# Optimization experiments

Measured on AMD Instinct MI355X. Metric: run time of the kernel, lower is better.

## Reference

```python
import jax, jax.numpy as jnp
import numpy as np

C = 512
HEADS = 8
B, H, W = 2, 64, 64


def setup_inputs() -> dict:
    key = jax.random.key(0)
    k1, k2, k3, k4, k5 = jax.random.split(key, 5)
    s = 1.0 / np.sqrt(C)
    return {
        "hidden_states": jax.random.normal(k1, (B, C, H, W), dtype=jnp.float32),
        "qkv_w": jax.random.normal(k2, (3 * C, C), dtype=jnp.float32) * s,
        "qkv_b": jax.random.normal(k3, (3 * C,), dtype=jnp.float32) * 0.02,
        "proj_w": jax.random.normal(k4, (C, C), dtype=jnp.float32) * s,
        "proj_b": jax.random.normal(k5, (C,), dtype=jnp.float32) * 0.02,
    }


def reference(hidden_states, qkv_w, qkv_b, proj_w, proj_b):
    b, c, h, w = hidden_states.shape
    n = h * w  # sequence length
    heads = HEADS
    dim_head = c // heads
    scale = dim_head ** -0.5

    x = hidden_states.reshape(b, c, n)  # [b, c, n]
    # 1x1 conv1d == matmul over channel dim
    qkv = jnp.einsum("oc,bcn->bon", qkv_w, x) + qkv_b[None, :, None]  # [b, 3c, n]
    q, k, v = jnp.split(qkv, 3, axis=1)
    # [b, heads, dim_head, n] -> [b, heads, n, dim_head]
    def split_heads(t):
        return t.reshape(b, heads, dim_head, n).transpose(0, 1, 3, 2)
    q, k, v = split_heads(q), split_heads(k), split_heads(v)

    attn = jnp.einsum("bhqd,bhkd->bhqk", q, k) * scale  # [b, heads, n, n]
    attn = jax.nn.softmax(attn, axis=-1)
    out = jnp.einsum("bhqk,bhkd->bhqd", attn, v)  # [b, heads, n, dim_head]
    out = out.transpose(0, 1, 3, 2).reshape(b, c, n)  # [b, c, n]
    out = jnp.einsum("oc,bcn->bon", proj_w, out) + proj_b[None, :, None]
    return out  # [b, c, h*w] (matches torch module, no reshape back)
```

## Files before the change

### kernel.cpp

```cpp
#include <hip/hip_runtime.h>


typedef __attribute__((ext_vector_type(8))) short s16x8;
typedef __attribute__((ext_vector_type(4))) float f32x4;
typedef __attribute__((ext_vector_type(16))) float f32x16;
typedef __attribute__((ext_vector_type(4))) unsigned short u16x4;
typedef __attribute__((ext_vector_type(2))) unsigned u32x2;
typedef __attribute__((ext_vector_type(4))) unsigned u32x4;

__device__ __forceinline__ unsigned short f2bf(float f) {
  unsigned u = __builtin_bit_cast(unsigned, f);
  u += 0x7fffu + ((u >> 16) & 1u);
  return (unsigned short)(u >> 16);
}

__device__ __forceinline__ float bf2f(short s) {
  return __builtin_bit_cast(float, ((unsigned)(unsigned short)s) << 16);
}

__device__ __forceinline__ unsigned cvt_pk_bf16(float lo, float hi) {
  unsigned r;
  asm("v_cvt_pk_bf16_f32 %0, %1, %2" : "=v"(r) : "v"(lo), "v"(hi));
  return r;
}

__global__ __launch_bounds__(256) void prep_weights(
    const float* __restrict__ qkv_w, const float* __restrict__ proj_w,
    short* __restrict__ wq, short* __restrict__ wp) {
  int t = blockIdx.x * 256 + threadIdx.x;
  const int NQ = 1536 * 512 / 4;
  if (t < NQ) {
    float4 v = ((const float4*)qkv_w)[t];
    u16x4 o; o[0] = f2bf(v.x); o[1] = f2bf(v.y); o[2] = f2bf(v.z); o[3] = f2bf(v.w);
    ((u16x4*)wq)[t] = o;
  } else {
    int t2 = t - NQ;
    float4 v = ((const float4*)proj_w)[t2];
    u16x4 o; o[0] = f2bf(v.x); o[1] = f2bf(v.y); o[2] = f2bf(v.z); o[3] = f2bf(v.w);
    ((u16x4*)wp)[t2] = o;
  }
}

__global__ __launch_bounds__(256) void prep_transpose(
    const float* __restrict__ x, short* __restrict__ xt) {
  __shared__ short TL[64 * 72];
  const int b = blockIdx.z, c0 = blockIdx.y * 64, n0 = blockIdx.x * 64;
  const int t = threadIdx.x;
  const int cr = t >> 4, n4 = (t & 15) * 4;
#pragma unroll
  for (int i = 0; i < 4; i++) {
    int c = cr + i * 16;
    float4 v = *(const float4*)(x + ((size_t)(b * 512 + c0 + c)) * 4096 + n0 + n4);
    TL[(n4 + 0) * 72 + c] = (short)f2bf(v.x);
    TL[(n4 + 1) * 72 + c] = (short)f2bf(v.y);
    TL[(n4 + 2) * 72 + c] = (short)f2bf(v.z);
    TL[(n4 + 3) * 72 + c] = (short)f2bf(v.w);
  }
  __syncthreads();
  const int n = t >> 2;
#pragma unroll
  for (int s2 = 0; s2 < 2; s2++) {
    int s = (t & 3) * 2 + s2;
    s16x8 v = *(const s16x8*)&TL[n * 72 + s * 8];
    *(s16x8*)(xt + ((size_t)(b * 4096 + n0 + n)) * 512 + c0 + s * 8) = v;
  }
}

__global__ __launch_bounds__(256) void qkv_gemm(
    const short* __restrict__ wq, const short* __restrict__ xt,
    const float* __restrict__ qkv_b,
    short* __restrict__ qkbuf,
    short* __restrict__ vbuf) {
  __shared__ short Al[128 * 40];
  __shared__ short Bl[128 * 40];
  const int b = blockIdx.z;
  const int m0 = blockIdx.y * 128, n0 = blockIdx.x * 128;
  const bool swapped = (blockIdx.y < 8);
  const int t = threadIdx.x, lane = t & 63, wid = t >> 6;
  const int wr = wid >> 1, wc = wid & 1;
  const int srow = t >> 1, scol = (t & 1) * 16;
  const short* gA = wq + (size_t)(m0 + srow) * 512 + scol;
  const short* gB = xt + ((size_t)(b * 4096 + n0 + srow)) * 512 + scol;
  short* lA = &Al[srow * 40 + scol];
  short* lB = &Bl[srow * 40 + scol];
  const short* As = swapped ? Bl : Al;
  const short* Bs = swapped ? Al : Bl;
  f32x4 acc[4][4] = {};
  for (int ks = 0; ks < 16; ks++) {
    *(s16x8*)lA       = *(const s16x8*)(gA + ks * 32);
    *(s16x8*)(lA + 8) = *(const s16x8*)(gA + ks * 32 + 8);
    *(s16x8*)lB       = *(const s16x8*)(gB + ks * 32);
    *(s16x8*)(lB + 8) = *(const s16x8*)(gB + ks * 32 + 8);
    __syncthreads();
    s16x8 af[4], bf[4];
#pragma unroll
    for (int i = 0; i < 4; i++) {
      af[i] = *(const s16x8*)&As[(wr * 64 + i * 16 + (lane & 15)) * 40 + ((lane >> 4) << 3)];
      bf[i] = *(const s16x8*)&Bs[(wc * 64 + i * 16 + (lane & 15)) * 40 + ((lane >> 4) << 3)];
    }
#pragma unroll
    for (int i = 0; i < 4; i++)
#pragma unroll
      for (int j = 0; j < 4; j++)
        acc[i][j] = __builtin_amdgcn_mfma_f32_16x16x32_bf16(af[i], bf[j], acc[i][j], 0, 0, 0);
    __syncthreads();
  }
  if (!swapped) {
#pragma unroll
    for (int i = 0; i < 4; i++)
#pragma unroll
      for (int r = 0; r < 4; r++) {
        int orow = m0 + wr * 64 + i * 16 + ((lane >> 4) << 2) + r;
        float bias = qkv_b[orow];
#pragma unroll
        for (int j = 0; j < 4; j++) {
          int ncol = n0 + wc * 64 + j * 16 + (lane & 15);
          vbuf[((size_t)(b * 512 + orow - 1024)) * 4096 + ncol] = (short)f2bf(acc[i][j][r] + bias);
        }
      }
  } else {
    const float qs = (m0 < 512) ? 0.18033688f : 1.0f;
#pragma unroll
    for (int j = 0; j < 4; j++) {
      int ocol = m0 + wc * 64 + j * 16 + (lane & 15);
      float bias = qkv_b[ocol];
#pragma unroll
      for (int i = 0; i < 4; i++)
#pragma unroll
        for (int r = 0; r < 4; r++) {
          int nrow = n0 + wr * 64 + i * 16 + ((lane >> 4) << 2) + r;
          qkbuf[((size_t)(b * 4096 + nrow)) * 1024 + ocol] = (short)f2bf((acc[i][j][r] + bias) * qs);
        }
    }
  }
}

__global__ __launch_bounds__(256) void flash_attn(
    const short* __restrict__ qkbuf, const short* __restrict__ vbuf,
    short* __restrict__ opart,
    float* __restrict__ mlbuf) {
  __shared__ short Kl[64 * 64];
  __shared__ short Vl[64 * 64];
  const int t = threadIdx.x, lane = t & 63, wid = t >> 6;
  const int hi = lane >> 5, q32 = lane & 31;
  const int j = blockIdx.x;
  const int lid = ((j & 7) << 7) + (j >> 3);
  const int bh = lid >> 6, b = bh >> 3, h = bh & 7;
  const int rest = lid & 63;
  const int qc = rest >> 1, half = rest & 1;
  const int qb = qc * 128 + wid * 32;
  const int kt0 = half * 32;

  s16x8 qf[4];
  {
    const short* qrow = qkbuf + ((size_t)(b * 4096 + qb + q32)) * 1024 + h * 64 + hi * 8;
#pragma unroll
    for (int dc = 0; dc < 4; dc++) qf[dc] = *(const s16x8*)(qrow + dc * 16);
  }

  f32x16 oacc[2] = {};
  float m = -__builtin_inff();
  float l = 0.f;

  const int srow = t >> 2;
  const int swz = (srow & 7) << 4;
  const int o0 = ((t & 3) * 32) ^ swz;
  const int o1 = ((t & 3) * 32 + 16) ^ swz;
  const short* gK = qkbuf + ((size_t)(b * 4096 + kt0 * 64 + srow)) * 1024 + 512 + h * 64 + (t & 3) * 16;
  const short* gV = vbuf + ((size_t)(b * 512 + h * 64 + srow)) * 4096 + kt0 * 64 + (t & 3) * 16;
  char* lKrow = (char*)&Kl[srow * 64];
  char* lVrow = (char*)&Vl[srow * 64];

  s16x8 pk0 = *(const s16x8*)gK, pk1 = *(const s16x8*)(gK + 8);
  s16x8 pv0 = *(const s16x8*)gV, pv1 = *(const s16x8*)(gV + 8);

  for (int kt = 0; kt < 32; kt++) {
    *(s16x8*)(lKrow + o0) = pk0;  *(s16x8*)(lKrow + o1) = pk1;
    *(s16x8*)(lVrow + o0) = pv0;  *(s16x8*)(lVrow + o1) = pv1;
    __syncthreads();
    if (kt < 31) {
      const short* nK = gK + (size_t)(kt + 1) * 64 * 1024;
      const short* nV = gV + (kt + 1) * 64;
      pk0 = *(const s16x8*)nK;  pk1 = *(const s16x8*)(nK + 8);
      pv0 = *(const s16x8*)nV;  pv1 = *(const s16x8*)(nV + 8);
    }
#pragma unroll
    for (int kb = 0; kb < 2; kb++) {
      f32x16 st = {};
      const int krow = kb * 32 + q32;
      const int ksw = (krow & 7) << 4;
#pragma unroll
      for (int dc = 0; dc < 4; dc++) {
        s16x8 kf = *(const s16x8*)((char*)&Kl[krow * 64] + ((dc * 32 + hi * 16) ^ ksw));
        st = __builtin_amdgcn_mfma_f32_32x32x16_bf16(kf, qf[dc], st, 0, 0, 0);
      }
      float x0 = fmaxf(st[0], st[1]),  x1 = fmaxf(st[2], st[3]);
      float x2 = fmaxf(st[4], st[5]),  x3 = fmaxf(st[6], st[7]);
      float x4 = fmaxf(st[8], st[9]),  x5 = fmaxf(st[10], st[11]);
      float x6 = fmaxf(st[12], st[13]), x7 = fmaxf(st[14], st[15]);
      x0 = fmaxf(x0, x1); x2 = fmaxf(x2, x3); x4 = fmaxf(x4, x5); x6 = fmaxf(x6, x7);
      x0 = fmaxf(x0, x2); x4 = fmaxf(x4, x6);
      float tm = fmaxf(x0, x4);
      tm = fmaxf(tm, __shfl_xor(tm, 32));
      if (!__all(tm <= m + 8.f)) {
        float mn = fmaxf(m, tm);
        float alpha = exp2f(m - mn);
        m = mn;
        l *= alpha;
#pragma unroll
        for (int di = 0; di < 2; di++)
#pragma unroll
          for (int r2 = 0; r2 < 16; r2++) oacc[di][r2] *= alpha;
      }
      float p[16];
      float ps = 0.f;
#pragma unroll
      for (int r2 = 0; r2 < 16; r2++) { p[r2] = exp2f(st[r2] - m); ps += p[r2]; }
      l += ps;
#pragma unroll
      for (int kh = 0; kh < 2; kh++) {
        unsigned A  = cvt_pk_bf16(p[kh * 8 + 0], p[kh * 8 + 1]);
        unsigned Bu = cvt_pk_bf16(p[kh * 8 + 4], p[kh * 8 + 5]);
        unsigned C  = cvt_pk_bf16(p[kh * 8 + 2], p[kh * 8 + 3]);
        unsigned D  = cvt_pk_bf16(p[kh * 8 + 6], p[kh * 8 + 7]);
        u32x2 r0 = __builtin_amdgcn_permlane32_swap(A, Bu, false, false);
        u32x2 r1 = __builtin_amdgcn_permlane32_swap(C, D, false, false);
        u32x4 uu; uu[0] = r0[0]; uu[1] = r1[0]; uu[2] = r0[1]; uu[3] = r1[1];
        s16x8 pf = __builtin_bit_cast(s16x8, uu);
#pragma unroll
        for (int di = 0; di < 2; di++) {
          const int vrow = di * 32 + q32;
          s16x8 vf = *(const s16x8*)((char*)&Vl[vrow * 64]
                       + ((kb * 64 + kh * 32 + hi * 16) ^ ((vrow & 7) << 4)));
          oacc[di] = __builtin_amdgcn_mfma_f32_32x32x16_bf16(vf, pf, oacc[di], 0, 0, 0);
        }
      }
    }
    __syncthreads();
  }
  l += __shfl_xor(l, 32);
  const size_t prow = ((size_t)(half * 16 + bh) * 4096 + qb + q32) * 64;
#pragma unroll
  for (int di = 0; di < 2; di++)
#pragma unroll
    for (int blk = 0; blk < 4; blk++) {
      uint2 w;
      w.x = cvt_pk_bf16(oacc[di][blk * 4 + 0], oacc[di][blk * 4 + 1]);
      w.y = cvt_pk_bf16(oacc[di][blk * 4 + 2], oacc[di][blk * 4 + 3]);
      *(uint2*)(opart + prow + di * 32 + blk * 8 + hi * 4) = w;
    }
  if (hi == 0) {
    const size_t mrow = (size_t)(half * 16 + bh) * 4096 + qb + q32;
    ((float2*)mlbuf)[mrow] = make_float2(m, l);
  }
}

__global__ __launch_bounds__(256) void merge_halves(
    const short* __restrict__ opart, const float* __restrict__ mlbuf,
    short* __restrict__ aout) {
  const int row = blockIdx.x * 256 + threadIdx.x;
  const int bh = row >> 12, q = row & 4095, b = bh >> 3, h = bh & 7;
  float2 ml0 = ((const float2*)mlbuf)[row];
  float2 ml1 = ((const float2*)mlbuf)[65536 + row];
  float mm = fmaxf(ml0.x, ml1.x);
  float w0 = exp2f(ml0.x - mm), w1 = exp2f(ml1.x - mm);
  float inv = 1.f / (w0 * ml0.y + w1 * ml1.y);
  w0 *= inv; w1 *= inv;
  const s16x8* r0 = (const s16x8*)(opart + (size_t)row * 64);
  const s16x8* r1 = (const s16x8*)(opart + ((size_t)65536 + row) * 64);
  short* po = aout + ((size_t)(b * 4096 + q)) * 512 + h * 64;
#pragma unroll
  for (int sg = 0; sg < 8; sg++) {
    s16x8 a0 = r0[sg], a1 = r1[sg];
    float v[8];
#pragma unroll
    for (int i = 0; i < 8; i++) v[i] = w0 * bf2f(a0[i]) + w1 * bf2f(a1[i]);
    u32x4 uu;
#pragma unroll
    for (int k = 0; k < 4; k++) uu[k] = cvt_pk_bf16(v[2 * k], v[2 * k + 1]);
    *(s16x8*)(po + sg * 8) = __builtin_bit_cast(s16x8, uu);
  }
}

__global__ __launch_bounds__(256) void proj_gemm(
    const short* __restrict__ wp, const short* __restrict__ aout,
    const float* __restrict__ proj_b, float* __restrict__ out) {
  __shared__ short Al[128 * 40];
  __shared__ short Bl[128 * 40];
  const int b = blockIdx.z;
  const int m0 = blockIdx.y * 128, n0 = blockIdx.x * 128;
  const int t = threadIdx.x, lane = t & 63, wid = t >> 6;
  const int wr = wid >> 1, wc = wid & 1;
  const int srow = t >> 1, scol = (t & 1) * 16;
  const short* gA = wp + (size_t)(m0 + srow) * 512 + scol;
  const short* gB = aout + ((size_t)(b * 4096 + n0 + srow)) * 512 + scol;
  short* lA = &Al[srow * 40 + scol];
  short* lB = &Bl[srow * 40 + scol];
  f32x4 acc[4][4] = {};
  for (int ks = 0; ks < 16; ks++) {
    *(s16x8*)lA       = *(const s16x8*)(gA + ks * 32);
    *(s16x8*)(lA + 8) = *(const s16x8*)(gA + ks * 32 + 8);
    *(s16x8*)lB       = *(const s16x8*)(gB + ks * 32);
    *(s16x8*)(lB + 8) = *(const s16x8*)(gB + ks * 32 + 8);
    __syncthreads();
    s16x8 af[4], bf[4];
#pragma unroll
    for (int i = 0; i < 4; i++) {
      af[i] = *(const s16x8*)&Al[(wr * 64 + i * 16 + (lane & 15)) * 40 + ((lane >> 4) << 3)];
      bf[i] = *(const s16x8*)&Bl[(wc * 64 + i * 16 + (lane & 15)) * 40 + ((lane >> 4) << 3)];
    }
#pragma unroll
    for (int i = 0; i < 4; i++)
#pragma unroll
      for (int j = 0; j < 4; j++)
        acc[i][j] = __builtin_amdgcn_mfma_f32_16x16x32_bf16(af[i], bf[j], acc[i][j], 0, 0, 0);
    __syncthreads();
  }
#pragma unroll
  for (int i = 0; i < 4; i++)
#pragma unroll
    for (int r = 0; r < 4; r++) {
      int orow = m0 + wr * 64 + i * 16 + ((lane >> 4) << 2) + r;
      float bias = proj_b[orow];
#pragma unroll
      for (int j = 0; j < 4; j++) {
        int ncol = n0 + wc * 64 + j * 16 + (lane & 15);
        out[((size_t)(b * 512 + orow)) * 4096 + ncol] = acc[i][j][r] + bias;
      }
    }
}

extern "C" void kernel_launch(void* const* d_in, const int* in_sizes, int n_in,
                              void* d_out, int out_size, void* d_ws, size_t ws_size,
                              hipStream_t stream) {
  const float* x      = (const float*)d_in[0];
  const float* qkv_w  = (const float*)d_in[1];
  const float* qkv_b  = (const float*)d_in[2];
  const float* proj_w = (const float*)d_in[3];
  const float* proj_b = (const float*)d_in[4];
  float* out = (float*)d_out;
  char* ws = (char*)d_ws;
  short* wq = (short*)(ws);
  short* wp = (short*)(ws + 1572864);
  short* xt = (short*)(ws + 2097152);
  short* qk = (short*)(ws + 10485760);
  short* vb = (short*)(ws + 27262976);
  short* ao = (short*)(ws + 35651584);
  short* op = (short*)(ws + 44040192);
  float* ml = (float*)(ws + 60817408);

  prep_weights  <<<1024, 256, 0, stream>>>(qkv_w, proj_w, wq, wp);
  prep_transpose<<<dim3(64, 8, 2), 256, 0, stream>>>(x, xt);
  qkv_gemm      <<<dim3(32, 12, 2), 256, 0, stream>>>(wq, xt, qkv_b, qk, vb);
  flash_attn    <<<1024, 256, 0, stream>>>(qk, vb, op, ml);
  merge_halves  <<<256, 256, 0, stream>>>(op, ml, ao);
  proj_gemm     <<<dim3(32, 4, 2), 256, 0, stream>>>(wp, ao, proj_b, out);
}
```

Measured before the change: 262.0 us.

## Double-buffer K/V tiles with direct global-to-LDS loads in flash attention

The flash-attention inner loop now fetches K and V tiles with global_load_lds straight into shared memory, instead of staging them through registers and then writing them to LDS. Two LDS buffers alternate, so the next tile's loads are issued while the current tile is being computed. The swizzle moves to the global source address, and the loop runs two tiles per iteration. s_setprio is raised around the MFMA sequences to favour matrix issue across waves. In exchange, LDS use doubles, which can lower occupancy, and correctness relies on the barrier waiting for the async loads to complete.

Measured after the change: 254.9 us. -2.7%, faster.

```diff
diff --git a/kernel.cpp b/kernel.cpp
--- a/kernel.cpp
+++ b/kernel.cpp
@@ -1,5 +1,7 @@
 #include <hip/hip_runtime.h>
 
+
+#include <stdint.h>
 
 typedef __attribute__((ext_vector_type(8))) short s16x8;
 typedef __attribute__((ext_vector_type(4))) float f32x4;
@@ -22,6 +24,14 @@
   unsigned r;
   asm("v_cvt_pk_bf16_f32 %0, %1, %2" : "=v"(r) : "v"(lo), "v"(hi));
   return r;
+}
+
+__device__ __forceinline__ void gl_lds16(const void* g, void* l) {
+  auto gp = reinterpret_cast<const __attribute__((address_space(1))) char*>(
+      reinterpret_cast<uintptr_t>(g));
+  auto lp = reinterpret_cast<__attribute__((address_space(3))) char*>(
+      reinterpret_cast<uintptr_t>(l));
+  __builtin_amdgcn_global_load_lds(gp, lp, 16, 0, 0);
 }
 
 __global__ __launch_bounds__(256) void prep_weights(
@@ -139,8 +149,8 @@
     const short* __restrict__ qkbuf, const short* __restrict__ vbuf,
     short* __restrict__ opart,
     float* __restrict__ mlbuf) {
-  __shared__ short Kl[64 * 64];
-  __shared__ short Vl[64 * 64];
+  __shared__ short Kl[2][64 * 64];
+  __shared__ short Vl[2][64 * 64];
   const int t = threadIdx.x, lane = t & 63, wid = t >> 6;
   const int hi = lane >> 5, q32 = lane & 31;
   const int j = blockIdx.x;
@@ -162,38 +172,38 @@
   float m = -__builtin_inff();
   float l = 0.f;
 
-  const int srow = t >> 2;
-  const int swz = (srow & 7) << 4;
-  const int o0 = ((t & 3) * 32) ^ swz;
-  const int o1 = ((t & 3) * 32 + 16) ^ swz;
-  const short* gK = qkbuf + ((size_t)(b * 4096 + kt0 * 64 + srow)) * 1024 + 512 + h * 64 + (t & 3) * 16;
-  const short* gV = vbuf + ((size_t)(b * 512 + h * 64 + srow)) * 4096 + kt0 * 64 + (t & 3) * 16;
-  char* lKrow = (char*)&Kl[srow * 64];
-  char* lVrow = (char*)&Vl[srow * 64];
-
-  s16x8 pk0 = *(const s16x8*)gK, pk1 = *(const s16x8*)(gK + 8);
-  s16x8 pv0 = *(const s16x8*)gV, pv1 = *(const s16x8*)(gV + 8);
-
-  for (int kt = 0; kt < 32; kt++) {
-    *(s16x8*)(lKrow + o0) = pk0;  *(s16x8*)(lKrow + o1) = pk1;
-    *(s16x8*)(lVrow + o0) = pv0;  *(s16x8*)(lVrow + o1) = pv1;
-    __syncthreads();
-    if (kt < 31) {
-      const short* nK = gK + (size_t)(kt + 1) * 64 * 1024;
-      const short* nV = gV + (kt + 1) * 64;
-      pk0 = *(const s16x8*)nK;  pk1 = *(const s16x8*)(nK + 8);
-      pv0 = *(const s16x8*)nV;  pv1 = *(const s16x8*)(nV + 8);
-    }
+  const int lrow = lane >> 3;
+  const int lcolb = ((lane & 7) << 4) ^ (lrow << 4);
+  const char* kp0 = (const char*)(qkbuf + ((size_t)(b * 4096 + kt0 * 64 + wid * 16 + lrow)) * 1024
+                                  + 512 + h * 64) + lcolb;
+  const char* kp1 = kp0 + 8 * 2048;
+  const char* vp0 = (const char*)(vbuf + ((size_t)(b * 512 + h * 64 + wid * 16 + lrow)) * 4096
+                                  + kt0 * 64) + lcolb;
+  const char* vp1 = vp0 + 8 * 8192;
+
+#define ISSUE_TILE(bi)                                                      \
+  do {                                                                      \
+    gl_lds16(kp0, &Kl[bi][(wid * 16 + 0) * 64]);                            \
+    gl_lds16(kp1, &Kl[bi][(wid * 16 + 8) * 64]);                            \
+    gl_lds16(vp0, &Vl[bi][(wid * 16 + 0) * 64]);                            \
+    gl_lds16(vp1, &Vl[bi][(wid * 16 + 8) * 64]);                            \
+    kp0 += 131072; kp1 += 131072; vp0 += 128; vp1 += 128;                   \
+  } while (0)
+
+  const int ksw = (q32 & 7) << 4;
+
+  auto do_tile = [&](const short* Klb, const short* Vlb) {
 #pragma unroll
     for (int kb = 0; kb < 2; kb++) {
       f32x16 st = {};
-      const int krow = kb * 32 + q32;
-      const int ksw = (krow & 7) << 4;
+      const char* kr = (const char*)(Klb + (kb * 32 + q32) * 64);
+      __builtin_amdgcn_s_setprio(1);
 #pragma unroll
       for (int dc = 0; dc < 4; dc++) {
-        s16x8 kf = *(const s16x8*)((char*)&Kl[krow * 64] + ((dc * 32 + hi * 16) ^ ksw));
+        s16x8 kf = *(const s16x8*)(kr + ((dc * 32 + hi * 16) ^ ksw));
         st = __builtin_amdgcn_mfma_f32_32x32x16_bf16(kf, qf[dc], st, 0, 0, 0);
       }
+      __builtin_amdgcn_s_setprio(0);
       float x0 = fmaxf(st[0], st[1]),  x1 = fmaxf(st[2], st[3]);
       float x2 = fmaxf(st[4], st[5]),  x3 = fmaxf(st[6], st[7]);
       float x4 = fmaxf(st[8], st[9]),  x5 = fmaxf(st[10], st[11]);
@@ -227,17 +237,30 @@
         u32x2 r1 = __builtin_amdgcn_permlane32_swap(C, D, false, false);
         u32x4 uu; uu[0] = r0[0]; uu[1] = r1[0]; uu[2] = r0[1]; uu[3] = r1[1];
         s16x8 pf = __builtin_bit_cast(s16x8, uu);
+        __builtin_amdgcn_s_setprio(1);
 #pragma unroll
         for (int di = 0; di < 2; di++) {
-          const int vrow = di * 32 + q32;
-          s16x8 vf = *(const s16x8*)((char*)&Vl[vrow * 64]
-                       + ((kb * 64 + kh * 32 + hi * 16) ^ ((vrow & 7) << 4)));
+          const char* vr = (const char*)(Vlb + (di * 32 + q32) * 64);
+          s16x8 vf = *(const s16x8*)(vr + ((kb * 64 + kh * 32 + hi * 16) ^ ksw));
           oacc[di] = __builtin_amdgcn_mfma_f32_32x32x16_bf16(vf, pf, oacc[di], 0, 0, 0);
         }
-      }
-    }
-    __syncthreads();
-  }
+        __builtin_amdgcn_s_setprio(0);
+      }
+    }
+  };
+
+  ISSUE_TILE(0);
+#pragma unroll 1
+  for (int it = 0; it < 16; it++) {
+    __syncthreads();
+    ISSUE_TILE(1);
+    do_tile(Kl[0], Vl[0]);
+    __syncthreads();
+    if (it < 15) ISSUE_TILE(0);
+    do_tile(Kl[1], Vl[1]);
+  }
+#undef ISSUE_TILE
+
   l += __shfl_xor(l, 32);
   const size_t prow = ((size_t)(half * 16 + bh) * 4096 + qb + q32) * 64;
 #pragma unroll
```
